# Performance work log

Hardware: AMD Instinct MI355X
Metric: run time of the kernel (lower is better)

Reference implementation:

```python
import jax, jax.numpy as jnp
import numpy as np

D_MODEL = 1024
N_HEADS = 16
D_FF = 4096
EPS = 1e-5


def layer_norm(x, gamma, beta):
    mu = jnp.mean(x, axis=-1, keepdims=True)
    var = jnp.mean(jnp.square(x - mu), axis=-1, keepdims=True)
    return (x - mu) * jax.lax.rsqrt(var + EPS) * gamma + beta


def setup_inputs() -> dict:
    key = jax.random.key(0)
    ks = jax.random.split(key, 12)
    C, F = D_MODEL, D_FF
    s = 1.0 / np.sqrt(C)
    sf = 1.0 / np.sqrt(F)
    return {
        "src": jax.random.normal(ks[0], (2, 2048, C), dtype=jnp.float32),
        "w_qkv": jax.random.uniform(ks[1], (3 * C, C), jnp.float32, -s, s),  # qkv_bias=False
        "w_proj": jax.random.uniform(ks[2], (C, C), jnp.float32, -s, s),
        "b_proj": jax.random.uniform(ks[3], (C,), jnp.float32, -s, s),
        "w1": jax.random.uniform(ks[4], (F, C), jnp.float32, -s, s),
        "b1": jax.random.uniform(ks[5], (F,), jnp.float32, -s, s),
        "w2": jax.random.uniform(ks[6], (C, F), jnp.float32, -sf, sf),
        "b2": jax.random.uniform(ks[7], (C,), jnp.float32, -sf, sf),
        "g1": jnp.ones((C,), jnp.float32),
        "be1": jnp.zeros((C,), jnp.float32),
        "g2": jnp.ones((C,), jnp.float32),
        "be2": jnp.zeros((C,), jnp.float32),
    }


def reference(src, w_qkv, w_proj, b_proj, w1, b1, w2, b2, g1, be1, g2, be2):
    B, N, C = src.shape
    H = N_HEADS
    D = C // H
    scale = D ** -0.5
    # --- self-attention (manual QK^T softmax) ---
    qkv = (src @ w_qkv.T).reshape(B, N, 3, H, D).transpose(2, 0, 3, 1, 4)  # [3,B,H,N,D]
    q, k, v = qkv[0], qkv[1], qkv[2]
    attn = jax.nn.softmax(jnp.einsum('bhnd,bhmd->bhnm', q, k) * scale, axis=-1)
    out = jnp.einsum('bhnm,bhmd->bhnd', attn, v).transpose(0, 2, 1, 3).reshape(B, N, C)
    out = out @ w_proj.T + b_proj
    # post-norm residual
    x = layer_norm(src + out, g1, be1)
    # --- FFN ---
    ff = jax.nn.relu(x @ w1.T + b1) @ w2.T + b2
    return layer_norm(x + ff, g2, be2)
```

## Files before the change

kernel.cpp:

```cpp
#include <hip/hip_runtime.h>
#include <hip/hip_bf16.h>
#include <stdint.h>

#define TOKENS 4096
#define SEQ    2048
#define CMODEL 1024
#define HEADS  16
#define HDIM   64
#define DFF    4096
#define NT     (SEQ / 64)

typedef __attribute__((ext_vector_type(8))) short     short8;
typedef __attribute__((ext_vector_type(8))) unsigned short ushort8;
typedef __attribute__((ext_vector_type(4))) unsigned short ushort4v;
typedef __attribute__((ext_vector_type(4))) float     f32x4;

typedef const __attribute__((address_space(1))) void gbl_cvoid;
typedef __attribute__((address_space(3))) void lds_void;

__device__ inline unsigned short f2bf(float f) {
  unsigned int u = __builtin_bit_cast(unsigned int, f);
  u += 0x7fffu + ((u >> 16) & 1u);
  return (unsigned short)(u >> 16);
}
__device__ inline float bf2f(unsigned short h) {
  unsigned int u = ((unsigned int)h) << 16;
  return __builtin_bit_cast(float, u);
}

__device__ inline void gload_lds16(const unsigned short* g, unsigned short* lds) {
  __builtin_amdgcn_global_load_lds((gbl_cvoid*)g, (lds_void*)lds, 16, 0, 0);
}

__global__ __launch_bounds__(256) void k_cvt(const float* __restrict__ in,
                                             unsigned short* __restrict__ out, int n8) {
  int i = blockIdx.x * 256 + threadIdx.x;
  if (i >= n8) return;
  const float4* p = (const float4*)in + 2 * (size_t)i;
  float4 a = p[0], b = p[1];
  ushort8 o;
  o[0] = f2bf(a.x); o[1] = f2bf(a.y); o[2] = f2bf(a.z); o[3] = f2bf(a.w);
  o[4] = f2bf(b.x); o[5] = f2bf(b.y); o[6] = f2bf(b.z); o[7] = f2bf(b.w);
  ((ushort8*)out)[i] = o;
}

template<int EPI>
__global__ __launch_bounds__(256) void k_gemm_bt(
    const unsigned short* __restrict__ A,
    const unsigned short* __restrict__ B,
    unsigned short* __restrict__ Cb,
    float* __restrict__ Cf,
    const float* __restrict__ bias,
    const float* __restrict__ resf,
    const unsigned short* __restrict__ resb,
    int M, int N, int K)
{
  __shared__ unsigned short As[2][128 * 32];
  __shared__ unsigned short Bs[2][128 * 32];
  const int t = threadIdx.x;
  const int lane = t & 63;
  const int w = t >> 6;
  const int wr = w >> 1, wc = w & 1;
  const int m0 = blockIdx.y * 128, n0 = blockIdx.x * 128;

  const int e0 = w * 1024 + lane * 8;
  const int e1 = e0 + 512;
  const int r0 = e0 >> 5, c0 = e0 & 31;
  const int r1 = e1 >> 5, c1 = e1 & 31;

  f32x4 acc[4][4] = {};
  const int lr = lane & 15, lh = lane >> 4;
  const int nkt = K >> 5;

  gload_lds16(A + (size_t)(m0 + r0) * K + c0, &As[0][w * 1024]);
  gload_lds16(A + (size_t)(m0 + r1) * K + c1, &As[0][w * 1024 + 512]);
  gload_lds16(B + (size_t)(n0 + r0) * K + c0, &Bs[0][w * 1024]);
  gload_lds16(B + (size_t)(n0 + r1) * K + c1, &Bs[0][w * 1024 + 512]);

  for (int kt = 0; kt < nkt; ++kt) {
    const int cur = kt & 1;
    if (kt + 1 < nkt) {
      const int kb = (kt + 1) << 5;
      gload_lds16(A + (size_t)(m0 + r0) * K + kb + c0, &As[cur ^ 1][w * 1024]);
      gload_lds16(A + (size_t)(m0 + r1) * K + kb + c1, &As[cur ^ 1][w * 1024 + 512]);
      gload_lds16(B + (size_t)(n0 + r0) * K + kb + c0, &Bs[cur ^ 1][w * 1024]);
      gload_lds16(B + (size_t)(n0 + r1) * K + kb + c1, &Bs[cur ^ 1][w * 1024 + 512]);
      asm volatile("s_waitcnt vmcnt(4)" ::: "memory");
    } else {
      asm volatile("s_waitcnt vmcnt(0)" ::: "memory");
    }
    __builtin_amdgcn_s_barrier();
    __builtin_amdgcn_sched_barrier(0);
    short8 af[4], bg[4];
    for (int m = 0; m < 4; ++m)
      af[m] = *(const short8*)&As[cur][(wr * 64 + m * 16 + lr) * 32 + lh * 8];
    for (int n = 0; n < 4; ++n)
      bg[n] = *(const short8*)&Bs[cur][(wc * 64 + n * 16 + lr) * 32 + lh * 8];
    for (int m = 0; m < 4; ++m)
      for (int n = 0; n < 4; ++n)
        acc[m][n] = __builtin_amdgcn_mfma_f32_16x16x32_bf16(af[m], bg[n], acc[m][n], 0, 0, 0);
    __builtin_amdgcn_s_barrier();
    __builtin_amdgcn_sched_barrier(0);
  }

  for (int m = 0; m < 4; ++m) {
    for (int n = 0; n < 4; ++n) {
      const int col = n0 + wc * 64 + n * 16 + lr;
      for (int r = 0; r < 4; ++r) {
        const int row = m0 + wr * 64 + m * 16 + lh * 4 + r;
        const size_t idx = (size_t)row * N + col;
        float v = acc[m][n][r];
        if (EPI == 0) {
          Cb[idx] = f2bf(v);
        } else if (EPI == 1) {
          Cf[idx] = v + bias[col] + resf[idx];
        } else if (EPI == 2) {
          v += bias[col];
          Cb[idx] = f2bf(v > 0.f ? v : 0.f);
        } else {
          Cf[idx] = v + bias[col] + bf2f(resb[idx]);
        }
      }
    }
  }
}

__global__ __launch_bounds__(256) void k_attn(
    const unsigned short* __restrict__ qkv,
    unsigned short* __restrict__ outb)
{
  __shared__ unsigned short Qs[64 * 64];
  __shared__ unsigned short Ks[2][64 * 64];
  __shared__ unsigned short Vt[2][64 * 64];
  __shared__ unsigned short Ps[4][16 * 72];

  const int t = threadIdx.x, lane = t & 63, w = t >> 6;
  const int bh = blockIdx.y;
  const int b = bh >> 4, h = bh & 15;
  const int q0 = blockIdx.x * 64;
  const size_t tokbase = (size_t)b * SEQ;
  const int qoff = h * 64, koff = 1024 + h * 64, voff = 2048 + h * 64;
  const int lr = lane & 15, lh = lane >> 4, lh4 = lh * 4;

  const int srow = lane >> 3;
  const int scol = (((lane & 7) ^ srow) & 7) << 3;

  gload_lds16(qkv + (tokbase + q0 + w * 16 + srow) * 3072 + qoff + scol, &Qs[w * 1024]);
  gload_lds16(qkv + (tokbase + q0 + w * 16 + 8 + srow) * 3072 + qoff + scol, &Qs[w * 1024 + 512]);
  gload_lds16(qkv + (tokbase + w * 16 + srow) * 3072 + koff + scol, &Ks[0][w * 1024]);
  gload_lds16(qkv + (tokbase + w * 16 + 8 + srow) * 3072 + koff + scol, &Ks[0][w * 1024 + 512]);

  const int kvr = t >> 2, d0v = (t & 3) * 16;
  const int vslotbase = (t & 3) * 2, kvslot = kvr >> 3, kvlow = kvr & 7;
  const int s0v = ((kvslot ^ vslotbase) & 7) << 3;
  const int s1v = ((kvslot ^ (vslotbase + 1)) & 7) << 3;

  ushort8 vA0, vA1, vB0, vB1;
  {
    const unsigned short* vsrc = qkv + (tokbase + kvr) * 3072 + voff + d0v;
    vA0 = *(const ushort8*)vsrc;
    vA1 = *(const ushort8*)(vsrc + 8);
  }
  asm volatile("s_waitcnt vmcnt(0)" ::: "memory");
  __builtin_amdgcn_s_barrier();
  __builtin_amdgcn_sched_barrier(0);

  const int qrow = w * 16 + lr;
  const short8 aq0 = *(const short8*)&Qs[qrow * 64 + (((lh ^ (lr & 7)) & 7) << 3)];
  const short8 aq1 = *(const short8*)&Qs[qrow * 64 + ((((lh + 4) ^ (lr & 7)) & 7) << 3)];

  int koffs0[4], koffs1[4], voffs0[4], voffs1[4];
  for (int nf = 0; nf < 4; ++nf) {
    const int krow = nf * 16 + lr;
    koffs0[nf] = krow * 64 + (((lh ^ (lr & 7)) & 7) << 3);
    koffs1[nf] = krow * 64 + ((((lh + 4) ^ (lr & 7)) & 7) << 3);
    const int d = nf * 16 + lr;
    const int key = (nf * 2 + (lr >> 3)) & 7;
    voffs0[nf] = d * 64 + (((lh ^ key) & 7) << 3);
    voffs1[nf] = d * 64 + ((((lh + 4) ^ key) & 7) << 3);
  }
  const unsigned short* pa0p = &Ps[w][lr * 72 + lh * 8];
  const unsigned short* pa1p = &Ps[w][lr * 72 + 32 + lh * 8];

  float m_run = -1e30f, l_run = 0.f;
  f32x4 oacc[4] = {};
  const float SCL = 0.125f * 1.44269504089f;

#define ATTN_STEP(CUR, VA0_, VA1_, VN0_, VN1_, KT)                                \
  {                                                                               \
    const int ktn = (KT) + 1;                                                     \
    if (ktn < NT) {                                                               \
      gload_lds16(qkv + (tokbase + ktn * 64 + w * 16 + srow) * 3072 + koff + scol,\
                  &Ks[1 - (CUR)][w * 1024]);                                      \
      gload_lds16(qkv + (tokbase + ktn * 64 + w * 16 + 8 + srow) * 3072 + koff + scol,\
                  &Ks[1 - (CUR)][w * 1024 + 512]);                                \
      const unsigned short* vsrc = qkv + (tokbase + ktn * 64 + kvr) * 3072 + voff + d0v;\
      VN0_ = *(const ushort8*)vsrc;                                               \
      VN1_ = *(const ushort8*)(vsrc + 8);                                         \
      asm volatile("s_waitcnt vmcnt(4)" ::: "memory");                            \
    } else {                                                                      \
      asm volatile("s_waitcnt vmcnt(0)" ::: "memory");                            \
    }                                                                             \
    __builtin_amdgcn_s_barrier();                                                 \
    __builtin_amdgcn_sched_barrier(0);                                            \
           \
    for (int i = 0; i < 8; ++i) Vt[CUR][(d0v + i) * 64 + s0v + kvlow] = VA0_[i];  \
    for (int i = 0; i < 8; ++i) Vt[CUR][(d0v + 8 + i) * 64 + s1v + kvlow] = VA1_[i];\
    f32x4 sacc[4] = {};                                                           \
    __builtin_amdgcn_s_setprio(1);                                                \
    for (int nf = 0; nf < 4; ++nf) {                                              \
      short8 bk0 = *(const short8*)&Ks[CUR][koffs0[nf]];                          \
      short8 bk1 = *(const short8*)&Ks[CUR][koffs1[nf]];                          \
      sacc[nf] = __builtin_amdgcn_mfma_f32_16x16x32_bf16(bk0, aq0, sacc[nf], 0, 0, 0);\
      sacc[nf] = __builtin_amdgcn_mfma_f32_16x16x32_bf16(bk1, aq1, sacc[nf], 0, 0, 0);\
    }                                                                             \
    __builtin_amdgcn_s_setprio(0);                                                \
                      \
    float tm = fmaxf(fmaxf(fmaxf(sacc[0][0], sacc[0][1]), fmaxf(sacc[0][2], sacc[0][3])),\
                     fmaxf(fmaxf(sacc[1][0], sacc[1][1]), fmaxf(sacc[1][2], sacc[1][3])));\
    tm = fmaxf(tm, fmaxf(fmaxf(fmaxf(sacc[2][0], sacc[2][1]), fmaxf(sacc[2][2], sacc[2][3])),\
                         fmaxf(fmaxf(sacc[3][0], sacc[3][1]), fmaxf(sacc[3][2], sacc[3][3]))));\
    tm *= SCL;                                                                    \
    tm = fmaxf(tm, __shfl_xor(tm, 16));                                           \
    tm = fmaxf(tm, __shfl_xor(tm, 32));                                           \
    if (__any(tm > m_run)) {                                                      \
      const float mnew = fmaxf(m_run, tm);                                        \
      const float alpha = exp2f(m_run - mnew);                                    \
      m_run = mnew; l_run *= alpha;                                               \
      const float ar0 = __shfl(alpha, lh4 + 0), ar1 = __shfl(alpha, lh4 + 1);     \
      const float ar2 = __shfl(alpha, lh4 + 2), ar3 = __shfl(alpha, lh4 + 3);     \
      for (int nf = 0; nf < 4; ++nf) {                                            \
        oacc[nf][0] *= ar0; oacc[nf][1] *= ar1;                                   \
        oacc[nf][2] *= ar2; oacc[nf][3] *= ar3;                                   \
      }                                                                           \
    }                                                                             \
    float rs = 0.f;                                                               \
    for (int nf = 0; nf < 4; ++nf) {                                              \
      float p0 = exp2f(__builtin_fmaf(sacc[nf][0], SCL, -m_run));                 \
      float p1 = exp2f(__builtin_fmaf(sacc[nf][1], SCL, -m_run));                 \
      float p2 = exp2f(__builtin_fmaf(sacc[nf][2], SCL, -m_run));                 \
      float p3 = exp2f(__builtin_fmaf(sacc[nf][3], SCL, -m_run));                 \
      rs += (p0 + p1) + (p2 + p3);                                                \
      uint2 pw;                                                                   \
      pw.x = (unsigned)f2bf(p0) | ((unsigned)f2bf(p1) << 16);                     \
      pw.y = (unsigned)f2bf(p2) | ((unsigned)f2bf(p3) << 16);                     \
      *(uint2*)&Ps[w][lr * 72 + nf * 16 + lh4] = pw;                              \
    }                                                                             \
    rs += __shfl_xor(rs, 16);                                                     \
    rs += __shfl_xor(rs, 32);                                                     \
    l_run += rs;                                                                  \
    short8 pa0 = *(const short8*)pa0p;                                            \
    short8 pa1 = *(const short8*)pa1p;                                            \
    asm volatile("s_waitcnt lgkmcnt(0)" ::: "memory");                            \
    __builtin_amdgcn_s_barrier();                                                 \
    __builtin_amdgcn_sched_barrier(0);                                            \
    __builtin_amdgcn_s_setprio(1);                                                \
    for (int nf = 0; nf < 4; ++nf) {                                              \
      short8 vb0 = *(const short8*)&Vt[CUR][voffs0[nf]];                          \
      short8 vb1 = *(const short8*)&Vt[CUR][voffs1[nf]];                          \
      oacc[nf] = __builtin_amdgcn_mfma_f32_16x16x32_bf16(pa0, vb0, oacc[nf], 0, 0, 0);\
      oacc[nf] = __builtin_amdgcn_mfma_f32_16x16x32_bf16(pa1, vb1, oacc[nf], 0, 0, 0);\
    }                                                                             \
    __builtin_amdgcn_s_setprio(0);                                                \
  }

  for (int kt2 = 0; kt2 < NT; kt2 += 2) {
    ATTN_STEP(0, vA0, vA1, vB0, vB1, kt2)
    ATTN_STEP(1, vB0, vB1, vA0, vA1, kt2 + 1)
  }
#undef ATTN_STEP

  const float lf0 = __shfl(l_run, lh4 + 0);
  const float lf1 = __shfl(l_run, lh4 + 1);
  const float lf2 = __shfl(l_run, lh4 + 2);
  const float lf3 = __shfl(l_run, lh4 + 3);
  const float ri0 = 1.f / lf0, ri1 = 1.f / lf1, ri2 = 1.f / lf2, ri3 = 1.f / lf3;
  for (int nf = 0; nf < 4; ++nf) {
    const int col = h * 64 + nf * 16 + lr;
    const size_t rowb = (tokbase + q0 + w * 16 + lh4) * (size_t)CMODEL + col;
    outb[rowb]               = f2bf(oacc[nf][0] * ri0);
    outb[rowb + CMODEL]      = f2bf(oacc[nf][1] * ri1);
    outb[rowb + 2 * CMODEL]  = f2bf(oacc[nf][2] * ri2);
    outb[rowb + 3 * CMODEL]  = f2bf(oacc[nf][3] * ri3);
  }
}

template<int OUT_BF>
__global__ __launch_bounds__(256) void k_ln(const float* __restrict__ in,
    const float* __restrict__ g, const float* __restrict__ b,
    float* __restrict__ outf, unsigned short* __restrict__ outb)
{
  const int row = blockIdx.x;
  const int t = threadIdx.x;
  const float4* x4 = (const float4*)(in + (size_t)row * CMODEL);
  float4 v = x4[t];
  float s  = v.x + v.y + v.z + v.w;
  float s2 = v.x * v.x + v.y * v.y + v.z * v.z + v.w * v.w;
  for (int off = 32; off; off >>= 1) { s += __shfl_down(s, off); s2 += __shfl_down(s2, off); }
  __shared__ float red[8];
  __shared__ float stats[2];
  const int wv = t >> 6;
  if ((t & 63) == 0) { red[wv] = s; red[4 + wv] = s2; }
  __syncthreads();
  if (t == 0) {
    float ts  = red[0] + red[1] + red[2] + red[3];
    float ts2 = red[4] + red[5] + red[6] + red[7];
    float mu  = ts * (1.f / CMODEL);
    float var = ts2 * (1.f / CMODEL) - mu * mu;
    stats[0] = mu; stats[1] = rsqrtf(var + 1e-5f);
  }
  __syncthreads();
  const float mu = stats[0], rstd = stats[1];
  float4 gv = ((const float4*)g)[t];
  float4 bv = ((const float4*)b)[t];
  float o0 = (v.x - mu) * rstd * gv.x + bv.x;
  float o1 = (v.y - mu) * rstd * gv.y + bv.y;
  float o2 = (v.z - mu) * rstd * gv.z + bv.z;
  float o3 = (v.w - mu) * rstd * gv.w + bv.w;
  if (OUT_BF) {
    ushort4v o; o[0] = f2bf(o0); o[1] = f2bf(o1); o[2] = f2bf(o2); o[3] = f2bf(o3);
    ((ushort4v*)(outb + (size_t)row * CMODEL))[t] = o;
  } else {
    float4 o; o.x = o0; o.y = o1; o.z = o2; o.w = o3;
    ((float4*)(outf + (size_t)row * CMODEL))[t] = o;
  }
}

extern "C" void kernel_launch(void* const* d_in, const int* in_sizes, int n_in,
                              void* d_out, int out_size, void* d_ws, size_t ws_size,
                              hipStream_t stream) {
  const float* src    = (const float*)d_in[0];
  const float* w_qkv  = (const float*)d_in[1];
  const float* w_proj = (const float*)d_in[2];
  const float* b_proj = (const float*)d_in[3];
  const float* w1     = (const float*)d_in[4];
  const float* b1     = (const float*)d_in[5];
  const float* w2     = (const float*)d_in[6];
  const float* b2     = (const float*)d_in[7];
  const float* g1     = (const float*)d_in[8];
  const float* be1    = (const float*)d_in[9];
  const float* g2     = (const float*)d_in[10];
  const float* be2    = (const float*)d_in[11];
  float* out = (float*)d_out;

  char* ws = (char*)d_ws;
  size_t off = 0;
  auto alloc = [&](size_t bytes) -> void* {
    void* p = ws + off;
    off += (bytes + 255) & ~(size_t)255;
    return p;
  };
  unsigned short* src_bf   = (unsigned short*)alloc((size_t)TOKENS * CMODEL * 2);
  unsigned short* wqkv_bf  = (unsigned short*)alloc((size_t)3 * CMODEL * CMODEL * 2);
  unsigned short* wproj_bf = (unsigned short*)alloc((size_t)CMODEL * CMODEL * 2);
  unsigned short* w1_bf    = (unsigned short*)alloc((size_t)DFF * CMODEL * 2);
  unsigned short* w2_bf    = (unsigned short*)alloc((size_t)CMODEL * DFF * 2);
  unsigned short* qkv_bf   = (unsigned short*)alloc((size_t)TOKENS * 3 * CMODEL * 2);
  unsigned short* attno_bf = (unsigned short*)alloc((size_t)TOKENS * CMODEL * 2);
  float*          z_f32    = (float*)alloc((size_t)TOKENS * CMODEL * 4);
  unsigned short* x_bf     = (unsigned short*)alloc((size_t)TOKENS * CMODEL * 2);
  unsigned short* h_bf     = (unsigned short*)alloc((size_t)TOKENS * DFF * 2);

  auto cvt = [&](const float* i, unsigned short* o, size_t n) {
    int n8 = (int)(n / 8);
    k_cvt<<<(n8 + 255) / 256, 256, 0, stream>>>(i, o, n8);
  };
  cvt(src,    src_bf,   (size_t)TOKENS * CMODEL);
  cvt(w_qkv,  wqkv_bf,  (size_t)3 * CMODEL * CMODEL);
  cvt(w_proj, wproj_bf, (size_t)CMODEL * CMODEL);
  cvt(w1,     w1_bf,    (size_t)DFF * CMODEL);
  cvt(w2,     w2_bf,    (size_t)CMODEL * DFF);

  k_gemm_bt<0><<<dim3(3072 / 128, TOKENS / 128), 256, 0, stream>>>(
      src_bf, wqkv_bf, qkv_bf, nullptr, nullptr, nullptr, nullptr, TOKENS, 3 * CMODEL, CMODEL);
  k_attn<<<dim3(SEQ / 64, 2 * HEADS), 256, 0, stream>>>(qkv_bf, attno_bf);
  k_gemm_bt<1><<<dim3(CMODEL / 128, TOKENS / 128), 256, 0, stream>>>(
      attno_bf, wproj_bf, nullptr, z_f32, b_proj, src, nullptr, TOKENS, CMODEL, CMODEL);
  k_ln<1><<<TOKENS, 256, 0, stream>>>(z_f32, g1, be1, nullptr, x_bf);
  k_gemm_bt<2><<<dim3(DFF / 128, TOKENS / 128), 256, 0, stream>>>(
      x_bf, w1_bf, h_bf, nullptr, b1, nullptr, nullptr, TOKENS, DFF, CMODEL);
  k_gemm_bt<3><<<dim3(CMODEL / 128, TOKENS / 128), 256, 0, stream>>>(
      h_bf, w2_bf, nullptr, z_f32, b2, nullptr, x_bf, TOKENS, CMODEL, DFF);
  k_ln<0><<<TOKENS, 256, 0, stream>>>(z_f32, g2, be2, out, nullptr);
}
```

Before: 445.4 us.

## Add 256x256 GEMM tiles, XCD-aware block swizzle, lazy softmax rescale, packed bf16 cvt

Adds a 512-thread 256x256-tile GEMM kernel for the QKV and FFN1 projections to raise data reuse per block, and remaps block IDs in the GEMMs and attention so neighbouring tiles land on the same XCD for L2 locality. The attention softmax now rescales only when the running max grows by more than 5 (in log2 units), uses a reshaped max-reduction tree, and converts probabilities with the hardware packed bf16 conversion instruction. The larger tiles use more LDS and registers and launch fewer blocks, which lowers occupancy. The lazy-rescale threshold lets exp values exceed 1, which carries some overflow and precision risk. The attention swizzle hardcodes the grid shape.

```diff
diff --git a/kernel.cpp b/kernel.cpp
--- a/kernel.cpp
+++ b/kernel.cpp
@@ -61,7 +61,11 @@
   const int lane = t & 63;
   const int w = t >> 6;
   const int wr = w >> 1, wc = w & 1;
-  const int m0 = blockIdx.y * 128, n0 = blockIdx.x * 128;
+  const int nwg = gridDim.x * gridDim.y;
+  const int bid = blockIdx.y * gridDim.x + blockIdx.x;
+  const int swz = (bid & 7) * (nwg >> 3) + (bid >> 3);
+  const int n0 = (swz % gridDim.x) * 128;
+  const int m0 = (swz / gridDim.x) * 128;
 
   const int e0 = w * 1024 + lane * 8;
   const int e1 = e0 + 512;
@@ -92,11 +96,15 @@
     __builtin_amdgcn_s_barrier();
     __builtin_amdgcn_sched_barrier(0);
     short8 af[4], bg[4];
+#pragma unroll
     for (int m = 0; m < 4; ++m)
       af[m] = *(const short8*)&As[cur][(wr * 64 + m * 16 + lr) * 32 + lh * 8];
+#pragma unroll
     for (int n = 0; n < 4; ++n)
       bg[n] = *(const short8*)&Bs[cur][(wc * 64 + n * 16 + lr) * 32 + lh * 8];
+#pragma unroll
     for (int m = 0; m < 4; ++m)
+#pragma unroll
       for (int n = 0; n < 4; ++n)
         acc[m][n] = __builtin_amdgcn_mfma_f32_16x16x32_bf16(af[m], bg[n], acc[m][n], 0, 0, 0);
     __builtin_amdgcn_s_barrier();
@@ -125,6 +133,88 @@
   }
 }
 
+template<int EPI>
+__global__ __launch_bounds__(512) void k_gemm256(
+    const unsigned short* __restrict__ A,
+    const unsigned short* __restrict__ B,
+    unsigned short* __restrict__ Cb,
+    const float* __restrict__ bias,
+    int M, int N, int K)
+{
+  __shared__ unsigned short As[2][256 * 32];
+  __shared__ unsigned short Bs[2][256 * 32];
+  const int t = threadIdx.x;
+  const int lane = t & 63;
+  const int w = t >> 6;
+  const int wr = w >> 2, wc = w & 3;
+  const int nwg = gridDim.x * gridDim.y;
+  const int bid = blockIdx.y * gridDim.x + blockIdx.x;
+  const int swz = (bid & 7) * (nwg >> 3) + (bid >> 3);
+  const int n0 = (swz % gridDim.x) * 256;
+  const int m0 = (swz / gridDim.x) * 256;
+
+  const int e0 = w * 1024 + lane * 8;
+  const int e1 = e0 + 512;
+  const int r0 = e0 >> 5, c0 = e0 & 31;
+  const int r1 = e1 >> 5, c1 = e1 & 31;
+
+  f32x4 acc[8][4] = {};
+  const int lr = lane & 15, lh = lane >> 4;
+  const int nkt = K >> 5;
+
+  gload_lds16(A + (size_t)(m0 + r0) * K + c0, &As[0][w * 1024]);
+  gload_lds16(A + (size_t)(m0 + r1) * K + c1, &As[0][w * 1024 + 512]);
+  gload_lds16(B + (size_t)(n0 + r0) * K + c0, &Bs[0][w * 1024]);
+  gload_lds16(B + (size_t)(n0 + r1) * K + c1, &Bs[0][w * 1024 + 512]);
+
+  for (int kt = 0; kt < nkt; ++kt) {
+    const int cur = kt & 1;
+    if (kt + 1 < nkt) {
+      const int kb = (kt + 1) << 5;
+      gload_lds16(A + (size_t)(m0 + r0) * K + kb + c0, &As[cur ^ 1][w * 1024]);
+      gload_lds16(A + (size_t)(m0 + r1) * K + kb + c1, &As[cur ^ 1][w * 1024 + 512]);
+      gload_lds16(B + (size_t)(n0 + r0) * K + kb + c0, &Bs[cur ^ 1][w * 1024]);
+      gload_lds16(B + (size_t)(n0 + r1) * K + kb + c1, &Bs[cur ^ 1][w * 1024 + 512]);
+      asm volatile("s_waitcnt vmcnt(4)" ::: "memory");
+    } else {
+      asm volatile("s_waitcnt vmcnt(0)" ::: "memory");
+    }
+    __builtin_amdgcn_s_barrier();
+    __builtin_amdgcn_sched_barrier(0);
+    short8 af[8], bg[4];
+#pragma unroll
+    for (int m = 0; m < 8; ++m)
+      af[m] = *(const short8*)&As[cur][(wr * 128 + m * 16 + lr) * 32 + lh * 8];
+#pragma unroll
+    for (int n = 0; n < 4; ++n)
+      bg[n] = *(const short8*)&Bs[cur][(wc * 64 + n * 16 + lr) * 32 + lh * 8];
+#pragma unroll
+    for (int m = 0; m < 8; ++m)
+#pragma unroll
+      for (int n = 0; n < 4; ++n)
+        acc[m][n] = __builtin_amdgcn_mfma_f32_16x16x32_bf16(af[m], bg[n], acc[m][n], 0, 0, 0);
+    __builtin_amdgcn_s_barrier();
+    __builtin_amdgcn_sched_barrier(0);
+  }
+
+  for (int m = 0; m < 8; ++m) {
+    for (int n = 0; n < 4; ++n) {
+      const int col = n0 + wc * 64 + n * 16 + lr;
+      for (int r = 0; r < 4; ++r) {
+        const int row = m0 + wr * 128 + m * 16 + lh * 4 + r;
+        const size_t idx = (size_t)row * N + col;
+        float v = acc[m][n][r];
+        if (EPI == 0) {
+          Cb[idx] = f2bf(v);
+        } else {
+          v += bias[col];
+          Cb[idx] = f2bf(v > 0.f ? v : 0.f);
+        }
+      }
+    }
+  }
+}
+
 __global__ __launch_bounds__(256) void k_attn(
     const unsigned short* __restrict__ qkv,
     unsigned short* __restrict__ outb)
@@ -135,9 +225,11 @@
   __shared__ unsigned short Ps[4][16 * 72];
 
   const int t = threadIdx.x, lane = t & 63, w = t >> 6;
-  const int bh = blockIdx.y;
+  const int bid0 = blockIdx.y * 32 + blockIdx.x;
+  const int swz = (bid0 & 7) * 128 + (bid0 >> 3);
+  const int bh = swz >> 5;
   const int b = bh >> 4, h = bh & 15;
-  const int q0 = blockIdx.x * 64;
+  const int q0 = (swz & 31) * 64;
   const size_t tokbase = (size_t)b * SEQ;
   const int qoff = h * 64, koff = 1024 + h * 64, voff = 2048 + h * 64;
   const int lr = lane & 15, lh = lane >> 4, lh4 = lh * 4;
@@ -203,7 +295,6 @@
     }                                                                             \
     __builtin_amdgcn_s_barrier();                                                 \
     __builtin_amdgcn_sched_barrier(0);                                            \
-           \
     for (int i = 0; i < 8; ++i) Vt[CUR][(d0v + i) * 64 + s0v + kvlow] = VA0_[i];  \
     for (int i = 0; i < 8; ++i) Vt[CUR][(d0v + 8 + i) * 64 + s1v + kvlow] = VA1_[i];\
     f32x4 sacc[4] = {};                                                           \
@@ -215,15 +306,17 @@
       sacc[nf] = __builtin_amdgcn_mfma_f32_16x16x32_bf16(bk1, aq1, sacc[nf], 0, 0, 0);\
     }                                                                             \
     __builtin_amdgcn_s_setprio(0);                                                \
-                      \
-    float tm = fmaxf(fmaxf(fmaxf(sacc[0][0], sacc[0][1]), fmaxf(sacc[0][2], sacc[0][3])),\
-                     fmaxf(fmaxf(sacc[1][0], sacc[1][1]), fmaxf(sacc[1][2], sacc[1][3])));\
-    tm = fmaxf(tm, fmaxf(fmaxf(fmaxf(sacc[2][0], sacc[2][1]), fmaxf(sacc[2][2], sacc[2][3])),\
-                         fmaxf(fmaxf(sacc[3][0], sacc[3][1]), fmaxf(sacc[3][2], sacc[3][3]))));\
+                          \
+    float a0 = fmaxf(fmaxf(sacc[0][0], sacc[0][1]), sacc[0][2]);                  \
+    float a1 = fmaxf(fmaxf(sacc[0][3], sacc[1][0]), sacc[1][1]);                  \
+    float a2 = fmaxf(fmaxf(sacc[1][2], sacc[1][3]), sacc[2][0]);                  \
+    float a3 = fmaxf(fmaxf(sacc[2][1], sacc[2][2]), sacc[2][3]);                  \
+    float a4 = fmaxf(fmaxf(sacc[3][0], sacc[3][1]), sacc[3][2]);                  \
+    float tm = fmaxf(fmaxf(fmaxf(a0, a1), fmaxf(a2, a3)), fmaxf(a4, sacc[3][3])); \
     tm *= SCL;                                                                    \
     tm = fmaxf(tm, __shfl_xor(tm, 16));                                           \
     tm = fmaxf(tm, __shfl_xor(tm, 32));                                           \
-    if (__any(tm > m_run)) {                                                      \
+    if (__any(tm > m_run + 5.f)) {               \
       const float mnew = fmaxf(m_run, tm);                                        \
       const float alpha = exp2f(m_run - mnew);                                    \
       m_run = mnew; l_run *= alpha;                                               \
@@ -241,9 +334,10 @@
       float p2 = exp2f(__builtin_fmaf(sacc[nf][2], SCL, -m_run));                 \
       float p3 = exp2f(__builtin_fmaf(sacc[nf][3], SCL, -m_run));                 \
       rs += (p0 + p1) + (p2 + p3);                                                \
-      uint2 pw;                                                                   \
-      pw.x = (unsigned)f2bf(p0) | ((unsigned)f2bf(p1) << 16);                     \
-      pw.y = (unsigned)f2bf(p2) | ((unsigned)f2bf(p3) << 16);                     \
+      unsigned pk0, pk1;                                                          \
+      asm("v_cvt_pk_bf16_f32 %0, %1, %2" : "=v"(pk0) : "v"(p0), "v"(p1));         \
+      asm("v_cvt_pk_bf16_f32 %0, %1, %2" : "=v"(pk1) : "v"(p2), "v"(p3));         \
+      uint2 pw; pw.x = pk0; pw.y = pk1;                                           \
       *(uint2*)&Ps[w][lr * 72 + nf * 16 + lh4] = pw;                              \
     }                                                                             \
     rs += __shfl_xor(rs, 16);                                                     \
@@ -371,14 +465,14 @@
   cvt(w1,     w1_bf,    (size_t)DFF * CMODEL);
   cvt(w2,     w2_bf,    (size_t)CMODEL * DFF);
 
-  k_gemm_bt<0><<<dim3(3072 / 128, TOKENS / 128), 256, 0, stream>>>(
-      src_bf, wqkv_bf, qkv_bf, nullptr, nullptr, nullptr, nullptr, TOKENS, 3 * CMODEL, CMODEL);
+  k_gemm256<0><<<dim3(3072 / 256, TOKENS / 256), 512, 0, stream>>>(
+      src_bf, wqkv_bf, qkv_bf, nullptr, TOKENS, 3 * CMODEL, CMODEL);
   k_attn<<<dim3(SEQ / 64, 2 * HEADS), 256, 0, stream>>>(qkv_bf, attno_bf);
   k_gemm_bt<1><<<dim3(CMODEL / 128, TOKENS / 128), 256, 0, stream>>>(
       attno_bf, wproj_bf, nullptr, z_f32, b_proj, src, nullptr, TOKENS, CMODEL, CMODEL);
   k_ln<1><<<TOKENS, 256, 0, stream>>>(z_f32, g1, be1, nullptr, x_bf);
-  k_gemm_bt<2><<<dim3(DFF / 128, TOKENS / 128), 256, 0, stream>>>(
-      x_bf, w1_bf, h_bf, nullptr, b1, nullptr, nullptr, TOKENS, DFF, CMODEL);
+  k_gemm256<2><<<dim3(DFF / 256, TOKENS / 256), 512, 0, stream>>>(
+      x_bf, w1_bf, h_bf, b1, TOKENS, DFF, CMODEL);
   k_gemm_bt<3><<<dim3(CMODEL / 128, TOKENS / 128), 256, 0, stream>>>(
       h_bf, w2_bf, nullptr, z_f32, b2, nullptr, x_bf, TOKENS, CMODEL, DFF);
   k_ln<0><<<TOKENS, 256, 0, stream>>>(z_f32, g2, be2, out, nullptr);
```

Result: no change. 437.1 us (-1.9%).

## Split-K proj/FFN2 GEMMs, triple-buffer loads, swizzle blocks, fuse conversions

Applied to the files above, without the earlier changes.

Merges the five fp32-to-bf16 conversion launches into one kernel. Moves the GEMM to a three-stage LDS pipeline with an XCD-aware block swizzle. The small-N projection and FFN2 GEMMs become split-K=2 with fp32 partials, and the bias and residual adds move into the layernorm kernels. Attention gets the same block swizzle, a lazy max-rescale threshold and packed bf16 conversion. The partial buffers alias the qkv region, and the extra partial write/read traffic and larger LDS footprint could lower occupancy.

```diff
diff --git a/kernel.cpp b/kernel.cpp
--- a/kernel.cpp
+++ b/kernel.cpp
@@ -32,16 +32,34 @@
   __builtin_amdgcn_global_load_lds((gbl_cvoid*)g, (lds_void*)lds, 16, 0, 0);
 }
 
-__global__ __launch_bounds__(256) void k_cvt(const float* __restrict__ in,
-                                             unsigned short* __restrict__ out, int n8) {
-  int i = blockIdx.x * 256 + threadIdx.x;
-  if (i >= n8) return;
-  const float4* p = (const float4*)in + 2 * (size_t)i;
+#define CVT_B0 524288
+#define CVT_B1 917504
+#define CVT_B2 1048576
+#define CVT_B3 1572864
+#define CVT_B4 2097152
+__global__ __launch_bounds__(256) void k_cvt_all(
+    const float* __restrict__ src, const float* __restrict__ wqkv,
+    const float* __restrict__ wproj, const float* __restrict__ w1,
+    const float* __restrict__ w2,
+    unsigned short* __restrict__ o_src, unsigned short* __restrict__ o_wqkv,
+    unsigned short* __restrict__ o_wproj, unsigned short* __restrict__ o_w1,
+    unsigned short* __restrict__ o_w2)
+{
+  const int i = blockIdx.x * 256 + threadIdx.x;
+  const float* in;
+  unsigned short* out;
+  int off;
+  if (i < CVT_B0)      { in = src;   out = o_src;   off = i; }
+  else if (i < CVT_B1) { in = wqkv;  out = o_wqkv;  off = i - CVT_B0; }
+  else if (i < CVT_B2) { in = wproj; out = o_wproj; off = i - CVT_B1; }
+  else if (i < CVT_B3) { in = w1;    out = o_w1;    off = i - CVT_B2; }
+  else                 { in = w2;    out = o_w2;    off = i - CVT_B3; }
+  const float4* p = (const float4*)in + 2 * (size_t)off;
   float4 a = p[0], b = p[1];
   ushort8 o;
   o[0] = f2bf(a.x); o[1] = f2bf(a.y); o[2] = f2bf(a.z); o[3] = f2bf(a.w);
   o[4] = f2bf(b.x); o[5] = f2bf(b.y); o[6] = f2bf(b.z); o[7] = f2bf(b.w);
-  ((ushort8*)out)[i] = o;
+  ((ushort8*)out)[off] = o;
 }
 
 template<int EPI>
@@ -51,17 +69,20 @@
     unsigned short* __restrict__ Cb,
     float* __restrict__ Cf,
     const float* __restrict__ bias,
-    const float* __restrict__ resf,
-    const unsigned short* __restrict__ resb,
-    int M, int N, int K)
+    int M, int N, int K, int kspan)
 {
-  __shared__ unsigned short As[2][128 * 32];
-  __shared__ unsigned short Bs[2][128 * 32];
+  __shared__ unsigned short As[3][128 * 32];
+  __shared__ unsigned short Bs[3][128 * 32];
   const int t = threadIdx.x;
   const int lane = t & 63;
   const int w = t >> 6;
   const int wr = w >> 1, wc = w & 1;
-  const int m0 = blockIdx.y * 128, n0 = blockIdx.x * 128;
+  const int nwg = gridDim.x * gridDim.y;
+  const int bid = blockIdx.y * gridDim.x + blockIdx.x;
+  const int swz = (bid & 7) * (nwg >> 3) + (bid >> 3);
+  const int n0 = (swz % gridDim.x) * 128;
+  const int m0 = (swz / gridDim.x) * 128;
+  const int kbase = blockIdx.z * kspan;
 
   const int e0 = w * 1024 + lane * 8;
   const int e1 = e0 + 512;
@@ -70,21 +91,25 @@
 
   f32x4 acc[4][4] = {};
   const int lr = lane & 15, lh = lane >> 4;
-  const int nkt = K >> 5;
-
-  gload_lds16(A + (size_t)(m0 + r0) * K + c0, &As[0][w * 1024]);
-  gload_lds16(A + (size_t)(m0 + r1) * K + c1, &As[0][w * 1024 + 512]);
-  gload_lds16(B + (size_t)(n0 + r0) * K + c0, &Bs[0][w * 1024]);
-  gload_lds16(B + (size_t)(n0 + r1) * K + c1, &Bs[0][w * 1024 + 512]);
-
+  const int nkt = kspan >> 5;
+
+  auto stage = [&](int kt, int buf) {
+    const int kb = kbase + (kt << 5);
+    gload_lds16(A + (size_t)(m0 + r0) * K + kb + c0, &As[buf][w * 1024]);
+    gload_lds16(A + (size_t)(m0 + r1) * K + kb + c1, &As[buf][w * 1024 + 512]);
+    gload_lds16(B + (size_t)(n0 + r0) * K + kb + c0, &Bs[buf][w * 1024]);
+    gload_lds16(B + (size_t)(n0 + r1) * K + kb + c1, &Bs[buf][w * 1024 + 512]);
+  };
+  stage(0, 0);
+  if (nkt > 1) stage(1, 1);
+
+  int buf = 0;
   for (int kt = 0; kt < nkt; ++kt) {
-    const int cur = kt & 1;
-    if (kt + 1 < nkt) {
-      const int kb = (kt + 1) << 5;
-      gload_lds16(A + (size_t)(m0 + r0) * K + kb + c0, &As[cur ^ 1][w * 1024]);
-      gload_lds16(A + (size_t)(m0 + r1) * K + kb + c1, &As[cur ^ 1][w * 1024 + 512]);
-      gload_lds16(B + (size_t)(n0 + r0) * K + kb + c0, &Bs[cur ^ 1][w * 1024]);
-      gload_lds16(B + (size_t)(n0 + r1) * K + kb + c1, &Bs[cur ^ 1][w * 1024 + 512]);
+    if (kt + 2 < nkt) {
+      const int nb = buf + 2 >= 3 ? buf - 1 : buf + 2;
+      stage(kt + 2, nb);
+      asm volatile("s_waitcnt vmcnt(8)" ::: "memory");
+    } else if (kt + 1 < nkt) {
       asm volatile("s_waitcnt vmcnt(4)" ::: "memory");
     } else {
       asm volatile("s_waitcnt vmcnt(0)" ::: "memory");
@@ -92,17 +117,23 @@
     __builtin_amdgcn_s_barrier();
     __builtin_amdgcn_sched_barrier(0);
     short8 af[4], bg[4];
+#pragma unroll
     for (int m = 0; m < 4; ++m)
-      af[m] = *(const short8*)&As[cur][(wr * 64 + m * 16 + lr) * 32 + lh * 8];
+      af[m] = *(const short8*)&As[buf][(wr * 64 + m * 16 + lr) * 32 + lh * 8];
+#pragma unroll
     for (int n = 0; n < 4; ++n)
-      bg[n] = *(const short8*)&Bs[cur][(wc * 64 + n * 16 + lr) * 32 + lh * 8];
+      bg[n] = *(const short8*)&Bs[buf][(wc * 64 + n * 16 + lr) * 32 + lh * 8];
+#pragma unroll
     for (int m = 0; m < 4; ++m)
+#pragma unroll
       for (int n = 0; n < 4; ++n)
         acc[m][n] = __builtin_amdgcn_mfma_f32_16x16x32_bf16(af[m], bg[n], acc[m][n], 0, 0, 0);
     __builtin_amdgcn_s_barrier();
     __builtin_amdgcn_sched_barrier(0);
-  }
-
+    buf = buf + 1 >= 3 ? 0 : buf + 1;
+  }
+
+  float* Cfp = (EPI == 4) ? Cf + (size_t)blockIdx.z * ((size_t)M * N) : Cf;
   for (int m = 0; m < 4; ++m) {
     for (int n = 0; n < 4; ++n) {
       const int col = n0 + wc * 64 + n * 16 + lr;
@@ -112,13 +143,11 @@
         float v = acc[m][n][r];
         if (EPI == 0) {
           Cb[idx] = f2bf(v);
-        } else if (EPI == 1) {
-          Cf[idx] = v + bias[col] + resf[idx];
         } else if (EPI == 2) {
           v += bias[col];
           Cb[idx] = f2bf(v > 0.f ? v : 0.f);
         } else {
-          Cf[idx] = v + bias[col] + bf2f(resb[idx]);
+          Cfp[idx] = v;
         }
       }
     }
@@ -135,9 +164,11 @@
   __shared__ unsigned short Ps[4][16 * 72];
 
   const int t = threadIdx.x, lane = t & 63, w = t >> 6;
-  const int bh = blockIdx.y;
+  const int bid0 = blockIdx.y * 32 + blockIdx.x;
+  const int swz = (bid0 & 7) * 128 + (bid0 >> 3);
+  const int bh = swz >> 5;
   const int b = bh >> 4, h = bh & 15;
-  const int q0 = blockIdx.x * 64;
+  const int q0 = (swz & 31) * 64;
   const size_t tokbase = (size_t)b * SEQ;
   const int qoff = h * 64, koff = 1024 + h * 64, voff = 2048 + h * 64;
   const int lr = lane & 15, lh = lane >> 4, lh4 = lh * 4;
@@ -203,7 +234,6 @@
     }                                                                             \
     __builtin_amdgcn_s_barrier();                                                 \
     __builtin_amdgcn_sched_barrier(0);                                            \
-           \
     for (int i = 0; i < 8; ++i) Vt[CUR][(d0v + i) * 64 + s0v + kvlow] = VA0_[i];  \
     for (int i = 0; i < 8; ++i) Vt[CUR][(d0v + 8 + i) * 64 + s1v + kvlow] = VA1_[i];\
     f32x4 sacc[4] = {};                                                           \
@@ -215,15 +245,16 @@
       sacc[nf] = __builtin_amdgcn_mfma_f32_16x16x32_bf16(bk1, aq1, sacc[nf], 0, 0, 0);\
     }                                                                             \
     __builtin_amdgcn_s_setprio(0);                                                \
-                      \
-    float tm = fmaxf(fmaxf(fmaxf(sacc[0][0], sacc[0][1]), fmaxf(sacc[0][2], sacc[0][3])),\
-                     fmaxf(fmaxf(sacc[1][0], sacc[1][1]), fmaxf(sacc[1][2], sacc[1][3])));\
-    tm = fmaxf(tm, fmaxf(fmaxf(fmaxf(sacc[2][0], sacc[2][1]), fmaxf(sacc[2][2], sacc[2][3])),\
-                         fmaxf(fmaxf(sacc[3][0], sacc[3][1]), fmaxf(sacc[3][2], sacc[3][3]))));\
+    float a0 = fmaxf(fmaxf(sacc[0][0], sacc[0][1]), sacc[0][2]);                  \
+    float a1 = fmaxf(fmaxf(sacc[0][3], sacc[1][0]), sacc[1][1]);                  \
+    float a2 = fmaxf(fmaxf(sacc[1][2], sacc[1][3]), sacc[2][0]);                  \
+    float a3 = fmaxf(fmaxf(sacc[2][1], sacc[2][2]), sacc[2][3]);                  \
+    float a4 = fmaxf(fmaxf(sacc[3][0], sacc[3][1]), sacc[3][2]);                  \
+    float tm = fmaxf(fmaxf(fmaxf(a0, a1), fmaxf(a2, a3)), fmaxf(a4, sacc[3][3])); \
     tm *= SCL;                                                                    \
     tm = fmaxf(tm, __shfl_xor(tm, 16));                                           \
     tm = fmaxf(tm, __shfl_xor(tm, 32));                                           \
-    if (__any(tm > m_run)) {                                                      \
+    if (__any(tm > m_run + 5.f)) {               \
       const float mnew = fmaxf(m_run, tm);                                        \
       const float alpha = exp2f(m_run - mnew);                                    \
       m_run = mnew; l_run *= alpha;                                               \
@@ -241,9 +272,10 @@
       float p2 = exp2f(__builtin_fmaf(sacc[nf][2], SCL, -m_run));                 \
       float p3 = exp2f(__builtin_fmaf(sacc[nf][3], SCL, -m_run));                 \
       rs += (p0 + p1) + (p2 + p3);                                                \
-      uint2 pw;                                                                   \
-      pw.x = (unsigned)f2bf(p0) | ((unsigned)f2bf(p1) << 16);                     \
-      pw.y = (unsigned)f2bf(p2) | ((unsigned)f2bf(p3) << 16);                     \
+      unsigned pk0, pk1;                                                          \
+      asm("v_cvt_pk_bf16_f32 %0, %1, %2" : "=v"(pk0) : "v"(p0), "v"(p1));         \
+      asm("v_cvt_pk_bf16_f32 %0, %1, %2" : "=v"(pk1) : "v"(p2), "v"(p3));         \
+      uint2 pw; pw.x = pk0; pw.y = pk1;                                           \
       *(uint2*)&Ps[w][lr * 72 + nf * 16 + lh4] = pw;                              \
     }                                                                             \
     rs += __shfl_xor(rs, 16);                                                     \
@@ -285,15 +317,24 @@
   }
 }
 
-template<int OUT_BF>
-__global__ __launch_bounds__(256) void k_ln(const float* __restrict__ in,
+__global__ __launch_bounds__(256) void k_ln1(
+    const float* __restrict__ p,
+    const float* __restrict__ src, const float* __restrict__ bias,
     const float* __restrict__ g, const float* __restrict__ b,
-    float* __restrict__ outf, unsigned short* __restrict__ outb)
+    unsigned short* __restrict__ xout)
 {
   const int row = blockIdx.x;
   const int t = threadIdx.x;
-  const float4* x4 = (const float4*)(in + (size_t)row * CMODEL);
-  float4 v = x4[t];
+  const size_t rb = (size_t)row * CMODEL;
+  const float4 a0 = ((const float4*)(p + rb))[t];
+  const float4 a1 = ((const float4*)(p + (size_t)TOKENS * CMODEL + rb))[t];
+  const float4 sv = ((const float4*)(src + rb))[t];
+  const float4 bb = ((const float4*)bias)[t];
+  float4 v;
+  v.x = a0.x + a1.x + sv.x + bb.x;
+  v.y = a0.y + a1.y + sv.y + bb.y;
+  v.z = a0.z + a1.z + sv.z + bb.z;
+  v.w = a0.w + a1.w + sv.w + bb.w;
   float s  = v.x + v.y + v.z + v.w;
   float s2 = v.x * v.x + v.y * v.y + v.z * v.z + v.w * v.w;
   for (int off = 32; off; off >>= 1) { s += __shfl_down(s, off); s2 += __shfl_down(s2, off); }
@@ -313,17 +354,57 @@
   const float mu = stats[0], rstd = stats[1];
   float4 gv = ((const float4*)g)[t];
   float4 bv = ((const float4*)b)[t];
-  float o0 = (v.x - mu) * rstd * gv.x + bv.x;
-  float o1 = (v.y - mu) * rstd * gv.y + bv.y;
-  float o2 = (v.z - mu) * rstd * gv.z + bv.z;
-  float o3 = (v.w - mu) * rstd * gv.w + bv.w;
-  if (OUT_BF) {
-    ushort4v o; o[0] = f2bf(o0); o[1] = f2bf(o1); o[2] = f2bf(o2); o[3] = f2bf(o3);
-    ((ushort4v*)(outb + (size_t)row * CMODEL))[t] = o;
-  } else {
-    float4 o; o.x = o0; o.y = o1; o.z = o2; o.w = o3;
-    ((float4*)(outf + (size_t)row * CMODEL))[t] = o;
-  }
+  ushort4v o;
+  o[0] = f2bf((v.x - mu) * rstd * gv.x + bv.x);
+  o[1] = f2bf((v.y - mu) * rstd * gv.y + bv.y);
+  o[2] = f2bf((v.z - mu) * rstd * gv.z + bv.z);
+  o[3] = f2bf((v.w - mu) * rstd * gv.w + bv.w);
+  ((ushort4v*)(xout + rb))[t] = o;
+}
+
+__global__ __launch_bounds__(256) void k_ln2(
+    const float* __restrict__ q,
+    const unsigned short* __restrict__ xres, const float* __restrict__ bias,
+    const float* __restrict__ g, const float* __restrict__ b,
+    float* __restrict__ out)
+{
+  const int row = blockIdx.x;
+  const int t = threadIdx.x;
+  const size_t rb = (size_t)row * CMODEL;
+  const float4 a0 = ((const float4*)(q + rb))[t];
+  const float4 a1 = ((const float4*)(q + (size_t)TOKENS * CMODEL + rb))[t];
+  const ushort4v xv = ((const ushort4v*)(xres + rb))[t];
+  const float4 bb = ((const float4*)bias)[t];
+  float4 v;
+  v.x = a0.x + a1.x + bf2f(xv[0]) + bb.x;
+  v.y = a0.y + a1.y + bf2f(xv[1]) + bb.y;
+  v.z = a0.z + a1.z + bf2f(xv[2]) + bb.z;
+  v.w = a0.w + a1.w + bf2f(xv[3]) + bb.w;
+  float s  = v.x + v.y + v.z + v.w;
+  float s2 = v.x * v.x + v.y * v.y + v.z * v.z + v.w * v.w;
+  for (int off = 32; off; off >>= 1) { s += __shfl_down(s, off); s2 += __shfl_down(s2, off); }
+  __shared__ float red[8];
+  __shared__ float stats[2];
+  const int wv = t >> 6;
+  if ((t & 63) == 0) { red[wv] = s; red[4 + wv] = s2; }
+  __syncthreads();
+  if (t == 0) {
+    float ts  = red[0] + red[1] + red[2] + red[3];
+    float ts2 = red[4] + red[5] + red[6] + red[7];
+    float mu  = ts * (1.f / CMODEL);
+    float var = ts2 * (1.f / CMODEL) - mu * mu;
+    stats[0] = mu; stats[1] = rsqrtf(var + 1e-5f);
+  }
+  __syncthreads();
+  const float mu = stats[0], rstd = stats[1];
+  float4 gv = ((const float4*)g)[t];
+  float4 bv = ((const float4*)b)[t];
+  float4 o;
+  o.x = (v.x - mu) * rstd * gv.x + bv.x;
+  o.y = (v.y - mu) * rstd * gv.y + bv.y;
+  o.z = (v.z - mu) * rstd * gv.z + bv.z;
+  o.w = (v.w - mu) * rstd * gv.w + bv.w;
+  ((float4*)(out + rb))[t] = o;
 }
 
 extern "C" void kernel_launch(void* const* d_in, const int* in_sizes, int n_in,
@@ -355,31 +436,25 @@
   unsigned short* wproj_bf = (unsigned short*)alloc((size_t)CMODEL * CMODEL * 2);
   unsigned short* w1_bf    = (unsigned short*)alloc((size_t)DFF * CMODEL * 2);
   unsigned short* w2_bf    = (unsigned short*)alloc((size_t)CMODEL * DFF * 2);
-  unsigned short* qkv_bf   = (unsigned short*)alloc((size_t)TOKENS * 3 * CMODEL * 2);
-  unsigned short* attno_bf = (unsigned short*)alloc((size_t)TOKENS * CMODEL * 2);
-  float*          z_f32    = (float*)alloc((size_t)TOKENS * CMODEL * 4);
   unsigned short* x_bf     = (unsigned short*)alloc((size_t)TOKENS * CMODEL * 2);
   unsigned short* h_bf     = (unsigned short*)alloc((size_t)TOKENS * DFF * 2);
-
-  auto cvt = [&](const float* i, unsigned short* o, size_t n) {
-    int n8 = (int)(n / 8);
-    k_cvt<<<(n8 + 255) / 256, 256, 0, stream>>>(i, o, n8);
-  };
-  cvt(src,    src_bf,   (size_t)TOKENS * CMODEL);
-  cvt(w_qkv,  wqkv_bf,  (size_t)3 * CMODEL * CMODEL);
-  cvt(w_proj, wproj_bf, (size_t)CMODEL * CMODEL);
-  cvt(w1,     w1_bf,    (size_t)DFF * CMODEL);
-  cvt(w2,     w2_bf,    (size_t)CMODEL * DFF);
-
+  char* regionR = (char*)alloc((size_t)64 * 1024 * 1024);
+  unsigned short* qkv_bf   = (unsigned short*)regionR;
+  unsigned short* attno_bf = (unsigned short*)(regionR + (size_t)TOKENS * 3 * CMODEL * 2);
+  float*          p_proj   = (float*)(regionR + (size_t)TOKENS * 3 * CMODEL * 2 + (size_t)TOKENS * CMODEL * 2);
+  float*          p_ffn2   = (float*)regionR;
+
+  k_cvt_all<<<CVT_B4 / 256, 256, 0, stream>>>(src, w_qkv, w_proj, w1, w2,
+      src_bf, wqkv_bf, wproj_bf, w1_bf, w2_bf);
   k_gemm_bt<0><<<dim3(3072 / 128, TOKENS / 128), 256, 0, stream>>>(
-      src_bf, wqkv_bf, qkv_bf, nullptr, nullptr, nullptr, nullptr, TOKENS, 3 * CMODEL, CMODEL);
+      src_bf, wqkv_bf, qkv_bf, nullptr, nullptr, TOKENS, 3 * CMODEL, CMODEL, CMODEL);
   k_attn<<<dim3(SEQ / 64, 2 * HEADS), 256, 0, stream>>>(qkv_bf, attno_bf);
-  k_gemm_bt<1><<<dim3(CMODEL / 128, TOKENS / 128), 256, 0, stream>>>(
-      attno_bf, wproj_bf, nullptr, z_f32, b_proj, src, nullptr, TOKENS, CMODEL, CMODEL);
-  k_ln<1><<<TOKENS, 256, 0, stream>>>(z_f32, g1, be1, nullptr, x_bf);
+  k_gemm_bt<4><<<dim3(CMODEL / 128, TOKENS / 128, 2), 256, 0, stream>>>(
+      attno_bf, wproj_bf, nullptr, p_proj, nullptr, TOKENS, CMODEL, CMODEL, CMODEL / 2);
+  k_ln1<<<TOKENS, 256, 0, stream>>>(p_proj, src, b_proj, g1, be1, x_bf);
   k_gemm_bt<2><<<dim3(DFF / 128, TOKENS / 128), 256, 0, stream>>>(
-      x_bf, w1_bf, h_bf, nullptr, b1, nullptr, nullptr, TOKENS, DFF, CMODEL);
-  k_gemm_bt<3><<<dim3(CMODEL / 128, TOKENS / 128), 256, 0, stream>>>(
-      h_bf, w2_bf, nullptr, z_f32, b2, nullptr, x_bf, TOKENS, CMODEL, DFF);
-  k_ln<0><<<TOKENS, 256, 0, stream>>>(z_f32, g2, be2, out, nullptr);
-}
+      x_bf, w1_bf, h_bf, nullptr, b1, TOKENS, DFF, CMODEL, CMODEL);
+  k_gemm_bt<4><<<dim3(CMODEL / 128, TOKENS / 128, 2), 256, 0, stream>>>(
+      h_bf, w2_bf, nullptr, p_ffn2, nullptr, TOKENS, CMODEL, DFF, DFF / 2);
+  k_ln2<<<TOKENS, 256, 0, stream>>>(p_ffn2, x_bf, b2, g2, be2, out);
+}
```

Result: faster. 393.3 us (-11.7%).
